# Performance work log

Measured on AMD Instinct MI355X. Metric: run time of the kernel, lower is better.

The kernel has to match this reference:

```python
import jax, jax.numpy as jnp
import numpy as np

B = 256
NO_A, NF_A = 64, 4   # class A: n_obj, n_field (all state fields)
NO_B, NF_B = 32, 3   # class B
NS = NF_A + NF_B     # total state fields = 7
DIN, DL, DG, DH = 128, 64, 64, 256
DGE = DG * NF_A + DG * NF_B          # 448 global encoding dim
DIN_A = DGE + DL * NF_A              # 704 decoder input dim, class A
DIN_B = DGE + DL * NF_B              # 640 decoder input dim, class B
NP = 2  # distribution params per field (mean, scale)


def lrelu(x):
    return jnp.where(x >= 0, x, 0.01 * x)


def setup_inputs() -> dict:
    key = jax.random.key(0)
    ks = iter(jax.random.split(key, 40))
    def rn(shape, s=1.0):
        return jax.random.normal(next(ks), shape, jnp.float32) * s
    def w(shape):
        return rn(shape, 0.05)
    def rb(shape):
        return jax.random.randint(next(ks), shape, 0, 2).astype(bool)
    inp = dict(
        x_A=rn((B, NO_A, NF_A, DIN)),
        x_B=rn((B, NO_B, NF_B, DIN)),
        global_mask=rb((B, NS, NF_A + NF_B)),
        local_mask_A=rb((B, NF_A, NF_A)),
        local_mask_B=rb((B, NF_B, NF_B)),
        objmask_A=rb((B, NO_A)),
        objmask_B=rb((B, NO_B)),
        enc_Wl_A=w((DIN, DL)), enc_bl_A=w((DL,)),
        enc_Wg_A=w((DIN, DG)), enc_bg_A=w((DG,)),
        enc_Wl_B=w((DIN, DL)), enc_bl_B=w((DL,)),
        enc_Wg_B=w((DIN, DG)), enc_bg_B=w((DG,)),
        dec_W1_A=w((NF_A, DIN_A, DH)), dec_b1_A=w((NF_A, DH)),
        dec_W2_A=w((NF_A, DH, DH)), dec_b2_A=w((NF_A, DH)),
        dec_Wp_A=w((NF_A, DH, NP)), dec_bp_A=w((NF_A, NP)),
        dec_W1_B=w((NF_B, DIN_B, DH)), dec_b1_B=w((NF_B, DH)),
        dec_W2_B=w((NF_B, DH, DH)), dec_b2_B=w((NF_B, DH)),
        dec_Wp_B=w((NF_B, DH, NP)), dec_bp_B=w((NF_B, NP)),
        rw_W1=w((DGE, DH)), rw_b1=w((DH,)),
        rw_W2=w((DH, DH)), rw_b2=w((DH,)),
        rw_W3=w((DH, 1)), rw_b3=w((1,)),
    )
    return inp


def encode_local(x, Wl, bl, attrmask):
    # x: (B, O, F, DIN) -> (B, O, S, F*DL), masked_retain over attrmask (B, S, F)
    h = jax.nn.relu(x @ Wl + bl)                                  # (B,O,F,DL)
    y = jnp.where(attrmask[:, None, :, :, None], h[:, :, None, :, :], 0.0)  # (B,O,S,F,DL)
    return y.reshape(y.shape[0], y.shape[1], y.shape[2], -1)


def encode_global(x, Wg, bg, attrmask, objmask):
    # x: (B, O, F, DIN), attrmask: (B, NS, F), objmask: (B, O)
    h = x @ Wg + bg                                               # (B,O,F,DG)
    h = jnp.where(objmask[:, :, None, None], h, 0.0)
    r = jax.nn.relu(jnp.sum(h, axis=1))                           # (B,F,DG) sum-pool over objects
    y = jnp.where(attrmask[:, :, :, None], r[:, None], 0.0)       # (B,NS,F,DG)
    y = jnp.concatenate([y, r[:, None]], axis=1)                  # (B,NS+1,F,DG)
    return y.reshape(y.shape[0], y.shape[1], -1)


def decode(x, W1, b1, W2, b2, Wp, bp):
    # x: (B, O, S, Din); per-field (s) decoders stacked on leading axis
    h = lrelu(jnp.einsum('bosi,sid->bosd', x, W1) + b1)
    h = lrelu(jnp.einsum('bosd,sde->bose', h, W2) + b2)
    return jnp.einsum('bose,sep->bosp', h, Wp) + bp               # (B,O,S,NP)


def reference(x_A, x_B, global_mask, local_mask_A, local_mask_B, objmask_A, objmask_B,
              enc_Wl_A, enc_bl_A, enc_Wg_A, enc_bg_A,
              enc_Wl_B, enc_bl_B, enc_Wg_B, enc_bg_B,
              dec_W1_A, dec_b1_A, dec_W2_A, dec_b2_A, dec_Wp_A, dec_bp_A,
              dec_W1_B, dec_b1_B, dec_W2_B, dec_b2_B, dec_Wp_B, dec_bp_B,
              rw_W1, rw_b1, rw_W2, rw_b2, rw_W3, rw_b3):
    g_A = encode_global(x_A, enc_Wg_A, enc_bg_A, global_mask[:, :, :NF_A], objmask_A)
    g_B = encode_global(x_B, enc_Wg_B, enc_bg_B, global_mask[:, :, NF_A:], objmask_B)
    G = jnp.concatenate([g_A, g_B], axis=2)                       # (B, NS+1, DGE)

    l_A = encode_local(x_A, enc_Wl_A, enc_bl_A, local_mask_A)     # (B,NO_A,NF_A,NF_A*DL)
    gs_A = jnp.broadcast_to(G[:, None, :NF_A, :], (B, NO_A, NF_A, DGE))
    out_A = decode(jnp.concatenate([l_A, gs_A], axis=3),
                   dec_W1_A, dec_b1_A, dec_W2_A, dec_b2_A, dec_Wp_A, dec_bp_A)

    l_B = encode_local(x_B, enc_Wl_B, enc_bl_B, local_mask_B)
    gs_B = jnp.broadcast_to(G[:, None, NF_A:NS, :], (B, NO_B, NF_B, DGE))
    out_B = decode(jnp.concatenate([l_B, gs_B], axis=3),
                   dec_W1_B, dec_b1_B, dec_W2_B, dec_b2_B, dec_Wp_B, dec_bp_B)

    h = lrelu(G[:, -1, :] @ rw_W1 + rw_b1)
    h = lrelu(h @ rw_W2 + rw_b2)
    reward = (h @ rw_W3 + rw_b3)[:, 0]                            # (B,)
    return out_A, out_B, reward
```

## Files before the change

kernel.cpp:

```cpp
#include <hip/hip_runtime.h>
#include <hip/hip_bf16.h>

constexpr int Bn   = 256;
constexpr int NOA  = 64, NFA = 4;
constexpr int NOB  = 32, NFB = 3;
constexpr int NS   = 7;
constexpr int DIN  = 128, DL = 64, DG = 64, DH = 256;
constexpr int DGE  = 448;
constexpr int DINA = 704;
constexpr int DINB = 640;

typedef short  short8v __attribute__((ext_vector_type(8)));
typedef float  f32x4   __attribute__((ext_vector_type(4)));

__device__ __forceinline__ unsigned short f2bf(float x) {
  union { float f; unsigned int u; } a; a.f = x;
  unsigned int r = a.u + 0x7fff + ((a.u >> 16) & 1);
  return (unsigned short)(r >> 16);
}


struct MidArgs {
  const float *xA, *xB, *WlA, *WlB, *blA, *blB;
  unsigned short *hlA, *hlB;
  const int *omA, *omB;
  const float *WgA, *bgA, *WgB, *bgB;
  float *rA, *rB;
  const float *W1A, *W1B, *W2A, *W2B;
  unsigned short *W1tA, *W1tB, *W1gtA, *W1gtB, *W2tA, *W2tB;
};

template<int F>
__device__ void hl_body(const float* __restrict__ x, const float* __restrict__ Wl,
                        const float* __restrict__ bl, unsigned short* __restrict__ hlf,
                        int m0, unsigned char* smem) {
  auto Asb = reinterpret_cast<unsigned short(*)[72]>(smem);
  auto Bsb = reinterpret_cast<unsigned short(*)[136]>(smem + 36864);
  float (*tile)[65] = reinterpret_cast<float(*)[65]>(smem);
  const int t = threadIdx.x, w = t >> 6, lane = t & 63;
  const int lr = lane & 15, lg = lane >> 4;
  constexpr int KB1 = 2 * F;

#pragma unroll
  for (int i = 0; i < 32; ++i) {
    int idx = t + i * 256;
    tile[idx >> 6][idx & 63] = Wl[idx];
  }
  __syncthreads();
#pragma unroll
  for (int i = 0; i < 32; ++i) {
    int idx = t + i * 256;
    int n = idx >> 7, k = idx & 127;
    Bsb[n][k] = f2bf(tile[k][n]);
  }
  __syncthreads();

  f32x4 acc[4][4] = {};
  for (int k0 = 0; k0 < DIN; k0 += 64) {
    const float* xp = x + (size_t)(m0 + t) * DIN + k0;
#pragma unroll
    for (int j = 0; j < 8; ++j) {
      float4 a = *(const float4*)(xp + j * 8);
      float4 b = *(const float4*)(xp + j * 8 + 4);
      union { short8v v; unsigned short e[8]; } u;
      u.e[0] = f2bf(a.x); u.e[1] = f2bf(a.y); u.e[2] = f2bf(a.z); u.e[3] = f2bf(a.w);
      u.e[4] = f2bf(b.x); u.e[5] = f2bf(b.y); u.e[6] = f2bf(b.z); u.e[7] = f2bf(b.w);
      *reinterpret_cast<short8v*>(&Asb[t][j * 8]) = u.v;
    }
#pragma unroll
    for (int ks = 0; ks < 2; ++ks) {
      short8v af[4], bf[4];
#pragma unroll
      for (int mi = 0; mi < 4; ++mi)
        af[mi] = *reinterpret_cast<const short8v*>(&Asb[w * 64 + mi * 16 + lr][ks * 32 + lg * 8]);
#pragma unroll
      for (int ni = 0; ni < 4; ++ni)
        bf[ni] = *reinterpret_cast<const short8v*>(&Bsb[ni * 16 + lr][k0 + ks * 32 + lg * 8]);
#pragma unroll
      for (int mi = 0; mi < 4; ++mi)
#pragma unroll
        for (int ni = 0; ni < 4; ++ni)
          acc[mi][ni] = __builtin_amdgcn_mfma_f32_16x16x32_bf16(
              af[mi], bf[ni], acc[mi][ni], 0, 0, 0);
    }
  }
#pragma unroll
  for (int mi = 0; mi < 4; ++mi)
#pragma unroll
    for (int ni = 0; ni < 4; ++ni)
#pragma unroll
      for (int reg = 0; reg < 4; ++reg) {
        int row = mi * 16 + lg * 4 + reg;
        int col = ni * 16 + lr;
        float v = fmaxf(acc[mi][ni][reg] + bl[col], 0.f);
        Asb[w * 64 + row][col] = f2bf(v);
      }
  const int mpb = m0 + w * 64;
#pragma unroll
  for (int j = 0; j < 8; ++j) {
    int c = lane + j * 64;
    int ml = c >> 3, dls = c & 7;
    int mp = mpb + ml;
    int mrow = mp / F, f = mp % F;
    int m6 = mrow >> 6, mi = (mrow >> 4) & 3, lr2 = mrow & 15;
    int kb = 2 * f + (dls >> 2), lg2 = dls & 3;
    size_t dst = ((((size_t)m6 * KB1 + kb) * 4 + mi) * 64 + (lg2 * 16 + lr2)) * 8;
    *reinterpret_cast<short8v*>(hlf + dst) =
        *reinterpret_cast<const short8v*>(&Asb[w * 64 + ml][dls * 8]);
  }
}

template<int O, int F>
__device__ void xsum_rg_body(const float* __restrict__ x, const int* __restrict__ om,
                             const float* __restrict__ Wg, const float* __restrict__ bg,
                             float* __restrict__ r, int b, unsigned char* smem) {
  float* xsm = reinterpret_cast<float*>(smem + 36864 + 17408);
  const int t = threadIdx.x, f = t >> 6, lane = t & 63;
  if (f >= F) return;
  unsigned long long bal = __ballot(lane < O && om[(size_t)b * O + lane] != 0);
  float cnt = (float)__popcll(bal);
  float a0 = 0.f, a1 = 0.f;
  const float* xb = x + ((size_t)b * O * F + f) * DIN + lane;
#pragma unroll 8
  for (int o = 0; o < O; ++o) {
    float m = (float)((bal >> o) & 1ull);
    a0 += m * xb[(size_t)o * F * DIN];
    a1 += m * xb[(size_t)o * F * DIN + 64];
  }
  xsm[f * 128 + lane] = a0;
  xsm[f * 128 + lane + 64] = a1;
  asm volatile("s_waitcnt lgkmcnt(0)" ::: "memory");
  float acc = 0.f;
  const float* wp = Wg + lane;
#pragma unroll 8
  for (int i = 0; i < DIN; ++i) acc += xsm[f * 128 + i] * wp[(size_t)i * DG];
  acc += cnt * bg[lane];
  r[((size_t)b * F + f) * DG + lane] = fmaxf(acc, 0.f);
}

__device__ void wtrans_tile(const float* __restrict__ src, unsigned short* __restrict__ dst,
                            int N, int DINc, int koff, int Kout,
                            int s, int kt, int nt, unsigned char* smem) {
  float (*tile)[65] = reinterpret_cast<float(*)[65]>(smem);
  const int t = threadIdx.x;
#pragma unroll
  for (int i = 0; i < 16; ++i) {
    int rr = (t >> 6) + i * 4, c = t & 63;
    tile[rr][c] = src[((size_t)s * DINc + koff + kt * 64 + rr) * N + nt * 64 + c];
  }
  __syncthreads();
#pragma unroll
  for (int i = 0; i < 2; ++i) {
    int cidx = t + i * 256;
    int n = cidx >> 3, kc = (cidx & 7) * 8;
    union { short8v v; unsigned short e[8]; } u;
#pragma unroll
    for (int j = 0; j < 8; ++j) u.e[j] = f2bf(tile[kc + j][n]);
    *reinterpret_cast<short8v*>(dst + ((size_t)s * N + nt * 64 + n) * Kout + kt * 64 + kc) = u.v;
  }
}

__device__ void wtrans_frag(const float* __restrict__ src, unsigned short* __restrict__ dst,
                            int DINc, int koff, int KB,
                            int s, int kt, int nt, unsigned char* smem) {
  float (*tile)[65] = reinterpret_cast<float(*)[65]>(smem);
  const int t = threadIdx.x;
#pragma unroll
  for (int i = 0; i < 16; ++i) {
    int rr = (t >> 6) + i * 4, c = t & 63;
    tile[rr][c] = src[((size_t)s * DINc + koff + kt * 64 + rr) * 256 + nt * 64 + c];
  }
  __syncthreads();
#pragma unroll
  for (int i = 0; i < 2; ++i) {
    int cidx = t + i * 256;
    int nl = cidx >> 3, kslot = cidx & 7;
    union { short8v v; unsigned short e[8]; } u;
#pragma unroll
    for (int j = 0; j < 8; ++j) u.e[j] = f2bf(tile[kslot * 8 + j][nl]);
    int kb = kt * 2 + (kslot >> 2);
    int lane = (kslot & 3) * 16 + (nl & 15);
    int nchunk = nt * 4 + (nl >> 4);
    *reinterpret_cast<short8v*>(
        dst + ((((size_t)s * KB + kb) * 16 + nchunk) * 64 + lane) * 8) = u.v;
  }
}

__global__ __launch_bounds__(256) void mid_kernel(MidArgs a) {
  __shared__ __align__(16) unsigned char smem[56320];
  const int bid = blockIdx.x;
  if (bid < 256) {
    hl_body<NFA>(a.xA, a.WlA, a.blA, a.hlA, bid * 256, smem);
    xsum_rg_body<NOA, NFA>(a.xA, a.omA, a.WgA, a.bgA, a.rA, bid, smem);
  } else if (bid < 352) {
    hl_body<NFB>(a.xB, a.WlB, a.blB, a.hlB, (bid - 256) * 256, smem);
  } else if (bid < 608) {
    xsum_rg_body<NOB, NFB>(a.xB, a.omB, a.WgB, a.bgB, a.rB, bid - 352, smem);
  } else {
    int r = bid - 608;
    if (r < 64)       { wtrans_frag(a.W1A, a.W1tA, DINA, 0, 8,
                                    r / 16, (r % 16) >> 2, r & 3, smem); }
    else if (r < 100) { r -= 64;  wtrans_frag(a.W1B, a.W1tB, DINB, 0, 6,
                                    r / 12, (r % 12) >> 2, r & 3, smem); }
    else if (r < 212) { r -= 100; wtrans_tile(a.W1A, a.W1gtA, 256, DINA, NFA * DL, DGE,
                                    r / 28, (r % 28) >> 2, r & 3, smem); }
    else if (r < 296) { r -= 212; wtrans_tile(a.W1B, a.W1gtB, 256, DINB, NFB * DL, DGE,
                                    r / 28, (r % 28) >> 2, r & 3, smem); }
    else if (r < 360) { r -= 296; wtrans_frag(a.W2A, a.W2tA, DH, 0, 8,
                                    r / 16, (r % 16) >> 2, r & 3, smem); }
    else              { r -= 360; wtrans_frag(a.W2B, a.W2tB, DH, 0, 8,
                                    r / 16, (r % 16) >> 2, r & 3, smem); }
  }
}

struct GprArgs {
  const float *rA, *rB; const int *gm;
  const unsigned short *W1gtA, *W1gtB;
  const float *b1A, *b1B;
  float *g1A, *g1B;
  const float *rwW1, *rwb1, *rwW2, *rwb2, *rwW3, *rwb3;
  float *outR;
};

__device__ void gpart_body(const GprArgs& a, int bx, int sg, unsigned char* smem) {
  auto Asb = reinterpret_cast<unsigned short(*)[72]>(smem);
  auto Bsb = reinterpret_cast<unsigned short(*)[72]>(smem + 9216);
  const int t = threadIdx.x, w = t >> 6, lane = t & 63;
  const int lr = lane & 15, lg = lane >> 4;
  const int m0 = bx * 64;
  const unsigned short* W1gt; const float* b1; float* g1; int S, sl;
  if (sg < NFA) { W1gt = a.W1gtA; b1 = a.b1A; g1 = a.g1A; S = NFA; sl = sg; }
  else          { W1gt = a.W1gtB; b1 = a.b1B; g1 = a.g1B; S = NFB; sl = sg - NFA; }

  f32x4 acc[4][4] = {};
  for (int kt = 0; kt < 7; ++kt) {
    __syncthreads();
    const int f = kt;
    const float* rsrc = (f < NFA) ? (a.rA + (size_t)f * DG) : (a.rB + (size_t)(f - NFA) * DG);
    const int rstride = (f < NFA) ? NFA * DG : NFB * DG;
#pragma unroll
    for (int i = 0; i < 2; ++i) {
      int c = t + i * 256;
      int row = c >> 3, kc = (c & 7) * 8;
      int b = m0 + row;
      float mk = (a.gm[((size_t)b * NS + sg) * NS + f] != 0) ? 1.f : 0.f;
      const float* rp = rsrc + (size_t)b * rstride + kc;
      union { short8v v; unsigned short e[8]; } u;
#pragma unroll
      for (int j = 0; j < 8; ++j) u.e[j] = f2bf(mk * rp[j]);
      *reinterpret_cast<short8v*>(&Asb[row][kc]) = u.v;
    }
#pragma unroll
    for (int i = 0; i < 8; ++i) {
      int c = t + i * 256;
      int n = c >> 3, kc = (c & 7) * 8;
      *reinterpret_cast<short8v*>(&Bsb[n][kc]) = *reinterpret_cast<const short8v*>(
          W1gt + ((size_t)sl * 256 + n) * DGE + kt * 64 + kc);
    }
    __syncthreads();
#pragma unroll
    for (int ks = 0; ks < 2; ++ks) {
      short8v af[4], bf[4];
#pragma unroll
      for (int mi = 0; mi < 4; ++mi)
        af[mi] = *reinterpret_cast<const short8v*>(&Asb[mi * 16 + lr][ks * 32 + lg * 8]);
#pragma unroll
      for (int ni = 0; ni < 4; ++ni)
        bf[ni] = *reinterpret_cast<const short8v*>(&Bsb[w * 64 + ni * 16 + lr][ks * 32 + lg * 8]);
#pragma unroll
      for (int mi = 0; mi < 4; ++mi)
#pragma unroll
        for (int ni = 0; ni < 4; ++ni)
          acc[mi][ni] = __builtin_amdgcn_mfma_f32_16x16x32_bf16(
              af[mi], bf[ni], acc[mi][ni], 0, 0, 0);
    }
  }
#pragma unroll
  for (int mi = 0; mi < 4; ++mi)
#pragma unroll
    for (int reg = 0; reg < 4; ++reg) {
      int b = m0 + mi * 16 + lg * 4 + reg;
#pragma unroll
      for (int ni = 0; ni < 4; ++ni) {
        int col = w * 64 + ni * 16 + lr;
        g1[((size_t)b * S + sl) * DH + col] = acc[mi][ni][reg] + b1[(size_t)sl * DH + col];
      }
    }
}

__device__ void reward_body(const GprArgs& a, int b, unsigned char* smem) {
  float* Gs = reinterpret_cast<float*>(smem);
  float* h1 = Gs + DGE;
  float* red = h1 + DH;
  const int t = threadIdx.x;
  for (int j = t; j < DGE; j += 256)
    Gs[j] = (j < NFA * DG) ? a.rA[((size_t)b * NFA + (j >> 6)) * DG + (j & 63)]
                           : a.rB[((size_t)b * NFB + ((j - NFA * DG) >> 6)) * DG + (j & 63)];
  __syncthreads();
  float acc = a.rwb1[t];
  for (int j = 0; j < DGE; ++j) acc += Gs[j] * a.rwW1[(size_t)j * DH + t];
  h1[t] = (acc >= 0.f) ? acc : 0.01f * acc;
  __syncthreads();
  acc = a.rwb2[t];
  for (int j = 0; j < DH; ++j) acc += h1[j] * a.rwW2[(size_t)j * DH + t];
  acc = (acc >= 0.f) ? acc : 0.01f * acc;
  red[t] = acc * a.rwW3[t];
  __syncthreads();
  for (int off = 128; off > 0; off >>= 1) {
    if (t < off) red[t] += red[t + off];
    __syncthreads();
  }
  if (t == 0) a.outR[b] = red[0] + a.rwb3[0];
}

__global__ __launch_bounds__(256) void gpr_kernel(GprArgs a) {
  __shared__ __align__(16) unsigned char smem[46080];
  const int bid = blockIdx.x;
  if (bid < 28) gpart_body(a, bid & 3, bid >> 2, smem);
  else          reward_body(a, bid - 28, smem);
}

struct DecArgs {
  const unsigned short *hlA, *hlB, *W1tA, *W1tB, *W2tA, *W2tB;
  const int *lmA, *lmB;
  const float *g1A, *g1B, *WpA, *WpB, *b2A, *b2B, *bpA, *bpB;
  float *outA, *outB;
};

template<int NO, int F>
__device__ __forceinline__ void dec_body(
    int mt, int s, unsigned short* h1s , float* red ,
    const unsigned short* __restrict__ hlf, const int* __restrict__ lm,
    const float* __restrict__ g1,
    const unsigned short* __restrict__ W1f, const unsigned short* __restrict__ W2f,
    const float* __restrict__ Wp, const float* __restrict__ b2,
    const float* __restrict__ bp, float* __restrict__ out) {
  constexpr int KB1 = 2 * F;
  const int t = threadIdx.x, w = t >> 6, lane = t & 63;
  const int lr = lane & 15, lg = lane >> 4;
  const int mh = w >> 2, nq = w & 3;
  const int m6 = mt * 2 + mh;
  const int m0 = mt * 128;

  unsigned mkl = 0, mkh = 0;
#pragma unroll
  for (int f = 0; f < F; ++f) {
    if (NO == 64) {
      unsigned bit = (lm[((size_t)m6 * F + s) * F + f] != 0) ? 1u : 0u;
      mkl |= bit << f; mkh |= bit << f;
    } else {
      int b0 = m6 * 2;
      if (lm[((size_t)b0 * F + s) * F + f])       mkl |= 1u << f;
      if (lm[((size_t)(b0 + 1) * F + s) * F + f]) mkh |= 1u << f;
    }
  }
  float g1r[2][4];
#pragma unroll
  for (int ni = 0; ni < 4; ++ni) {
    int col = nq * 64 + ni * 16 + lr;
    if (NO == 64) {
      g1r[0][ni] = g1[((size_t)m6 * F + s) * DH + col];
      g1r[1][ni] = g1r[0][ni];
    } else {
      g1r[0][ni] = g1[((size_t)(m6 * 2) * F + s) * DH + col];
      g1r[1][ni] = g1[((size_t)(m6 * 2 + 1) * F + s) * DH + col];
    }
  }

  f32x4 acc[4][4] = {};
  const short8v zero8 = {0, 0, 0, 0, 0, 0, 0, 0};

  const unsigned short* Afb = hlf + (size_t)m6 * KB1 * 2048 + lane * 8;
  const unsigned short* B1b = W1f + ((size_t)s * KB1 * 16 + nq * 4) * 512 + lane * 8;
#pragma unroll
  for (int kb = 0; kb < KB1; ++kb) {
    const int f = kb >> 1;
    const bool okl = (mkl >> f) & 1, okh = (mkh >> f) & 1;
    const unsigned short* ab = Afb + (size_t)kb * 2048;
    const unsigned short* bb = B1b + (size_t)kb * 8192;
    short8v af[4], bf[4];
#pragma unroll
    for (int mi = 0; mi < 4; ++mi) {
      const bool ok = (mi < 2) ? okl : okh;
      const unsigned short* p = ok ? (ab + mi * 512) : bb;
      af[mi] = *reinterpret_cast<const short8v*>(p);
    }
#pragma unroll
    for (int ni = 0; ni < 4; ++ni)
      bf[ni] = *reinterpret_cast<const short8v*>(bb + ni * 512);
#pragma unroll
    for (int mi = 0; mi < 4; ++mi) {
      const bool ok = (mi < 2) ? okl : okh;
      af[mi] = ok ? af[mi] : zero8;
    }
#pragma unroll
    for (int mi = 0; mi < 4; ++mi)
#pragma unroll
      for (int ni = 0; ni < 4; ++ni)
        acc[mi][ni] = __builtin_amdgcn_mfma_f32_16x16x32_bf16(
            af[mi], bf[ni], acc[mi][ni], 0, 0, 0);
  }

#pragma unroll
  for (int mi = 0; mi < 4; ++mi) {
    int gi = (NO == 32) ? (mi >> 1) : 0;
#pragma unroll
    for (int reg = 0; reg < 4; ++reg) {
      int row = mh * 64 + mi * 16 + lg * 4 + reg;
#pragma unroll
      for (int ni = 0; ni < 4; ++ni) {
        int col = nq * 64 + ni * 16 + lr;
        float v = acc[mi][ni][reg] + g1r[gi][ni];
        v = (v >= 0.f) ? v : 0.01f * v;
        h1s[row * 264 + col] = f2bf(v);
        acc[mi][ni][reg] = 0.f;
      }
    }
  }
  __syncthreads();

  const unsigned short* B2b = W2f + ((size_t)s * 8 * 16 + nq * 4) * 512 + lane * 8;
#pragma unroll
  for (int kb = 0; kb < 8; ++kb) {
    short8v af[4], bf[4];
#pragma unroll
    for (int mi = 0; mi < 4; ++mi)
      af[mi] = *reinterpret_cast<const short8v*>(
          h1s + (mh * 64 + mi * 16 + lr) * 264 + kb * 32 + lg * 8);
#pragma unroll
    for (int ni = 0; ni < 4; ++ni)
      bf[ni] = *reinterpret_cast<const short8v*>(B2b + (size_t)kb * 8192 + ni * 512);
#pragma unroll
    for (int mi = 0; mi < 4; ++mi)
#pragma unroll
      for (int ni = 0; ni < 4; ++ni)
        acc[mi][ni] = __builtin_amdgcn_mfma_f32_16x16x32_bf16(
            af[mi], bf[ni], acc[mi][ni], 0, 0, 0);
  }

  float part[4][4][2] = {};
  const float* Wps = Wp + (size_t)s * DH * 2;
  const float* b2s = b2 + (size_t)s * DH;
#pragma unroll
  for (int ni = 0; ni < 4; ++ni) {
    int col = nq * 64 + ni * 16 + lr;
    float wp0 = Wps[col * 2 + 0], wp1 = Wps[col * 2 + 1], bb2 = b2s[col];
#pragma unroll
    for (int mi = 0; mi < 4; ++mi)
#pragma unroll
      for (int reg = 0; reg < 4; ++reg) {
        float v = acc[mi][ni][reg] + bb2;
        v = (v >= 0.f) ? v : 0.01f * v;
        part[mi][reg][0] += v * wp0;
        part[mi][reg][1] += v * wp1;
      }
  }
#pragma unroll
  for (int off = 1; off < 16; off <<= 1)
#pragma unroll
    for (int mi = 0; mi < 4; ++mi)
#pragma unroll
      for (int reg = 0; reg < 4; ++reg) {
        part[mi][reg][0] += __shfl_xor(part[mi][reg][0], off, 64);
        part[mi][reg][1] += __shfl_xor(part[mi][reg][1], off, 64);
      }
  if (lr == 0)
#pragma unroll
    for (int mi = 0; mi < 4; ++mi)
#pragma unroll
      for (int reg = 0; reg < 4; ++reg) {
        int rowin = mi * 16 + lg * 4 + reg;
        red[((size_t)w * 64 + rowin) * 2 + 0] = part[mi][reg][0];
        red[((size_t)w * 64 + rowin) * 2 + 1] = part[mi][reg][1];
      }
  __syncthreads();
  if (t < 256) {
    int row = t >> 1, p = t & 1;
    int mhr = row >> 6, rowin = row & 63;
    float sum = 0.f;
#pragma unroll
    for (int q = 0; q < 4; ++q)
      sum += red[((size_t)(mhr * 4 + q) * 64 + rowin) * 2 + p];
    out[((size_t)(m0 + row) * F + s) * 2 + p] = sum + bp[(size_t)s * 2 + p];
  }
}

__global__ __launch_bounds__(512, 4) void dec_kernel(DecArgs a) {
  __shared__ __align__(16) unsigned short h1s[128 * 264];
  __shared__ float red[1024];
  const int bid = blockIdx.x;
  if (bid < 512) {
    dec_body<NOA, NFA>(bid & 127, bid >> 7, h1s, red, a.hlA, a.lmA, a.g1A,
                       a.W1tA, a.W2tA, a.WpA, a.b2A, a.bpA, a.outA);
  } else {
    int r = bid - 512;
    dec_body<NOB, NFB>(r & 63, r >> 6, h1s, red, a.hlB, a.lmB, a.g1B,
                       a.W1tB, a.W2tB, a.WpB, a.b2B, a.bpB, a.outB);
  }
}

extern "C" void kernel_launch(void* const* d_in, const int* in_sizes, int n_in,
                              void* d_out, int out_size, void* d_ws, size_t ws_size,
                              hipStream_t stream) {
  const float* x_A  = (const float*)d_in[0];
  const float* x_B  = (const float*)d_in[1];
  const int*   gm   = (const int*)d_in[2];
  const int*   lmA  = (const int*)d_in[3];
  const int*   lmB  = (const int*)d_in[4];
  const int*   omA  = (const int*)d_in[5];
  const int*   omB  = (const int*)d_in[6];
  const float* Wl_A = (const float*)d_in[7];
  const float* bl_A = (const float*)d_in[8];
  const float* Wg_A = (const float*)d_in[9];
  const float* bg_A = (const float*)d_in[10];
  const float* Wl_B = (const float*)d_in[11];
  const float* bl_B = (const float*)d_in[12];
  const float* Wg_B = (const float*)d_in[13];
  const float* bg_B = (const float*)d_in[14];
  const float* W1_A = (const float*)d_in[15];
  const float* b1_A = (const float*)d_in[16];
  const float* W2_A = (const float*)d_in[17];
  const float* b2_A = (const float*)d_in[18];
  const float* Wp_A = (const float*)d_in[19];
  const float* bp_A = (const float*)d_in[20];
  const float* W1_B = (const float*)d_in[21];
  const float* b1_B = (const float*)d_in[22];
  const float* W2_B = (const float*)d_in[23];
  const float* b2_B = (const float*)d_in[24];
  const float* Wp_B = (const float*)d_in[25];
  const float* bp_B = (const float*)d_in[26];
  const float* rwW1 = (const float*)d_in[27];
  const float* rwb1 = (const float*)d_in[28];
  const float* rwW2 = (const float*)d_in[29];
  const float* rwb2 = (const float*)d_in[30];
  const float* rwW3 = (const float*)d_in[31];
  const float* rwb3 = (const float*)d_in[32];

  float* ws   = (float*)d_ws;
  float* rA   = ws;
  float* rB   = rA + 65536;
  float* g1A  = rB + 49152;
  float* g1B  = g1A + 262144;
  unsigned short* us    = (unsigned short*)(g1B + 196608);
  unsigned short* hlA   = us;
  unsigned short* hlB   = hlA + 4194304;
  unsigned short* W1tA  = hlB + 1572864;
  unsigned short* W1tB  = W1tA + 262144;
  unsigned short* W2tA  = W1tB + 147456;
  unsigned short* W2tB  = W2tA + 262144;
  unsigned short* W1gtA = W2tB + 196608;
  unsigned short* W1gtB = W1gtA + 458752;

  float* outA = (float*)d_out;
  float* outB = outA + 131072;
  float* outR = outA + 180224;

  MidArgs m;
  m.xA = x_A; m.xB = x_B; m.WlA = Wl_A; m.WlB = Wl_B; m.blA = bl_A; m.blB = bl_B;
  m.hlA = hlA; m.hlB = hlB; m.omA = omA; m.omB = omB;
  m.WgA = Wg_A; m.bgA = bg_A; m.WgB = Wg_B; m.bgB = bg_B;
  m.rA = rA; m.rB = rB;
  m.W1A = W1_A; m.W1B = W1_B; m.W2A = W2_A; m.W2B = W2_B;
  m.W1tA = W1tA; m.W1tB = W1tB; m.W1gtA = W1gtA; m.W1gtB = W1gtB;
  m.W2tA = W2tA; m.W2tB = W2tB;

  GprArgs g;
  g.rA = rA; g.rB = rB; g.gm = gm; g.W1gtA = W1gtA; g.W1gtB = W1gtB;
  g.b1A = b1_A; g.b1B = b1_B; g.g1A = g1A; g.g1B = g1B;
  g.rwW1 = rwW1; g.rwb1 = rwb1; g.rwW2 = rwW2; g.rwb2 = rwb2;
  g.rwW3 = rwW3; g.rwb3 = rwb3; g.outR = outR;

  DecArgs d;
  d.hlA = hlA; d.hlB = hlB; d.W1tA = W1tA; d.W1tB = W1tB;
  d.W2tA = W2tA; d.W2tB = W2tB; d.lmA = lmA; d.lmB = lmB;
  d.g1A = g1A; d.g1B = g1B; d.WpA = Wp_A; d.WpB = Wp_B;
  d.b2A = b2_A; d.b2B = b2_B; d.bpA = bp_A; d.bpB = bp_B;
  d.outA = outA; d.outB = outB;

  mid_kernel<<<1016, 256, 0, stream>>>(m);
  gpr_kernel<<<284, 256, 0, stream>>>(g);
  dec_kernel<<<704, 512, 0, stream>>>(d);
}
```

Before: 88.80 us.

## Stage decoder GEMM1 tiles via direct global-to-LDS loads and halve h1 buffer

The first decoder GEMM now stages its A and B tiles into shared memory with global_load_lds, so the eight waves share one copy of the W1 tile instead of each loading its own fragments from global memory. The second GEMM is split into two phases, one per half of the waves, so the h1 staging buffer only needs 64 rows and total LDS per block shrinks. This aims to cut redundant global traffic and raise occupancy. In exchange it adds a __syncthreads per k-step and leaves half the waves idle in each GEMM2 phase, which serialises that stage.

```diff
diff --git a/kernel.cpp b/kernel.cpp
--- a/kernel.cpp
+++ b/kernel.cpp
@@ -17,6 +17,12 @@
   union { float f; unsigned int u; } a; a.f = x;
   unsigned int r = a.u + 0x7fff + ((a.u >> 16) & 1);
   return (unsigned short)(r >> 16);
+}
+
+__device__ __forceinline__ void gload_lds16(const void* g, void* l) {
+  __builtin_amdgcn_global_load_lds(
+      (const __attribute__((address_space(1))) void*)g,
+      (__attribute__((address_space(3))) void*)l, 16, 0, 0);
 }
 
 
@@ -329,7 +335,9 @@
 
 template<int NO, int F>
 __device__ __forceinline__ void dec_body(
-    int mt, int s, unsigned short* h1s , float* red ,
+    int mt, int s,
+    unsigned short* h1s , unsigned short* Ast ,
+    unsigned short* Bst ,
     const unsigned short* __restrict__ hlf, const int* __restrict__ lm,
     const float* __restrict__ g1,
     const unsigned short* __restrict__ W1f, const unsigned short* __restrict__ W2f,
@@ -370,74 +378,83 @@
   f32x4 acc[4][4] = {};
   const short8v zero8 = {0, 0, 0, 0, 0, 0, 0, 0};
 
-  const unsigned short* Afb = hlf + (size_t)m6 * KB1 * 2048 + lane * 8;
-  const unsigned short* B1b = W1f + ((size_t)s * KB1 * 16 + nq * 4) * 512 + lane * 8;
+  const int m6s = mt * 2 + (t >> 8);
 #pragma unroll
   for (int kb = 0; kb < KB1; ++kb) {
+    gload_lds16(hlf + ((size_t)m6s * KB1 + kb) * 2048 + (t & 255) * 8, Ast + t * 8);
+    const unsigned short* bbase = W1f + ((size_t)s * KB1 + kb) * 8192;
+    gload_lds16(bbase + t * 8,         Bst + t * 8);
+    gload_lds16(bbase + (t + 512) * 8, Bst + (t + 512) * 8);
+    __syncthreads();
+
     const int f = kb >> 1;
     const bool okl = (mkl >> f) & 1, okh = (mkh >> f) & 1;
-    const unsigned short* ab = Afb + (size_t)kb * 2048;
-    const unsigned short* bb = B1b + (size_t)kb * 8192;
     short8v af[4], bf[4];
 #pragma unroll
-    for (int mi = 0; mi < 4; ++mi) {
-      const bool ok = (mi < 2) ? okl : okh;
-      const unsigned short* p = ok ? (ab + mi * 512) : bb;
-      af[mi] = *reinterpret_cast<const short8v*>(p);
-    }
-#pragma unroll
-    for (int ni = 0; ni < 4; ++ni)
-      bf[ni] = *reinterpret_cast<const short8v*>(bb + ni * 512);
+    for (int mi = 0; mi < 4; ++mi)
+      af[mi] = *reinterpret_cast<const short8v*>(Ast + mh * 2048 + mi * 512 + lane * 8);
 #pragma unroll
     for (int mi = 0; mi < 4; ++mi) {
       const bool ok = (mi < 2) ? okl : okh;
       af[mi] = ok ? af[mi] : zero8;
     }
 #pragma unroll
+    for (int ni = 0; ni < 4; ++ni)
+      bf[ni] = *reinterpret_cast<const short8v*>(Bst + ((nq * 4 + ni) * 64 + lane) * 8);
+#pragma unroll
     for (int mi = 0; mi < 4; ++mi)
 #pragma unroll
       for (int ni = 0; ni < 4; ++ni)
         acc[mi][ni] = __builtin_amdgcn_mfma_f32_16x16x32_bf16(
             af[mi], bf[ni], acc[mi][ni], 0, 0, 0);
-  }
-
-#pragma unroll
-  for (int mi = 0; mi < 4; ++mi) {
-    int gi = (NO == 32) ? (mi >> 1) : 0;
-#pragma unroll
-    for (int reg = 0; reg < 4; ++reg) {
-      int row = mh * 64 + mi * 16 + lg * 4 + reg;
-#pragma unroll
-      for (int ni = 0; ni < 4; ++ni) {
-        int col = nq * 64 + ni * 16 + lr;
-        float v = acc[mi][ni][reg] + g1r[gi][ni];
-        v = (v >= 0.f) ? v : 0.01f * v;
-        h1s[row * 264 + col] = f2bf(v);
-        acc[mi][ni][reg] = 0.f;
+    __syncthreads();
+  }
+
+  const unsigned short* B2b = W2f + ((size_t)s * 8 * 16 + nq * 4) * 512 + lane * 8;
+#pragma unroll
+  for (int ph = 0; ph < 2; ++ph) {
+    if (mh == ph) {
+#pragma unroll
+      for (int mi = 0; mi < 4; ++mi) {
+        int gi = (NO == 32) ? (mi >> 1) : 0;
+#pragma unroll
+        for (int reg = 0; reg < 4; ++reg) {
+          int lrow = mi * 16 + lg * 4 + reg;
+#pragma unroll
+          for (int ni = 0; ni < 4; ++ni) {
+            int col = nq * 64 + ni * 16 + lr;
+            float v = acc[mi][ni][reg] + g1r[gi][ni];
+            v = (v >= 0.f) ? v : 0.01f * v;
+            h1s[lrow * 264 + col] = f2bf(v);
+            acc[mi][ni][reg] = 0.f;
+          }
+        }
       }
     }
-  }
-  __syncthreads();
-
-  const unsigned short* B2b = W2f + ((size_t)s * 8 * 16 + nq * 4) * 512 + lane * 8;
-#pragma unroll
-  for (int kb = 0; kb < 8; ++kb) {
-    short8v af[4], bf[4];
-#pragma unroll
-    for (int mi = 0; mi < 4; ++mi)
-      af[mi] = *reinterpret_cast<const short8v*>(
-          h1s + (mh * 64 + mi * 16 + lr) * 264 + kb * 32 + lg * 8);
-#pragma unroll
-    for (int ni = 0; ni < 4; ++ni)
-      bf[ni] = *reinterpret_cast<const short8v*>(B2b + (size_t)kb * 8192 + ni * 512);
-#pragma unroll
-    for (int mi = 0; mi < 4; ++mi)
-#pragma unroll
-      for (int ni = 0; ni < 4; ++ni)
-        acc[mi][ni] = __builtin_amdgcn_mfma_f32_16x16x32_bf16(
-            af[mi], bf[ni], acc[mi][ni], 0, 0, 0);
-  }
-
+    __syncthreads();
+    if (mh == ph) {
+#pragma unroll
+      for (int kb = 0; kb < 8; ++kb) {
+        short8v af[4], bf[4];
+#pragma unroll
+        for (int mi = 0; mi < 4; ++mi)
+          af[mi] = *reinterpret_cast<const short8v*>(
+              h1s + (mi * 16 + lr) * 264 + kb * 32 + lg * 8);
+#pragma unroll
+        for (int ni = 0; ni < 4; ++ni)
+          bf[ni] = *reinterpret_cast<const short8v*>(B2b + (size_t)kb * 8192 + ni * 512);
+#pragma unroll
+        for (int mi = 0; mi < 4; ++mi)
+#pragma unroll
+          for (int ni = 0; ni < 4; ++ni)
+            acc[mi][ni] = __builtin_amdgcn_mfma_f32_16x16x32_bf16(
+                af[mi], bf[ni], acc[mi][ni], 0, 0, 0);
+      }
+    }
+    __syncthreads();
+  }
+
+  float* red = reinterpret_cast<float*>(Ast);
   float part[4][4][2] = {};
   const float* Wps = Wp + (size_t)s * DH * 2;
   const float* b2s = b2 + (size_t)s * DH;
@@ -486,15 +503,16 @@
 }
 
 __global__ __launch_bounds__(512, 4) void dec_kernel(DecArgs a) {
-  __shared__ __align__(16) unsigned short h1s[128 * 264];
-  __shared__ float red[1024];
+  __shared__ __align__(16) unsigned short h1s[64 * 264];
+  __shared__ __align__(16) unsigned short Ast[4096];
+  __shared__ __align__(16) unsigned short Bst[8192];
   const int bid = blockIdx.x;
   if (bid < 512) {
-    dec_body<NOA, NFA>(bid & 127, bid >> 7, h1s, red, a.hlA, a.lmA, a.g1A,
+    dec_body<NOA, NFA>(bid & 127, bid >> 7, h1s, Ast, Bst, a.hlA, a.lmA, a.g1A,
                        a.W1tA, a.W2tA, a.WpA, a.b2A, a.bpA, a.outA);
   } else {
     int r = bid - 512;
-    dec_body<NOB, NFB>(r & 63, r >> 6, h1s, red, a.hlB, a.lmB, a.g1B,
+    dec_body<NOB, NFB>(r & 63, r >> 6, h1s, Ast, Bst, a.hlB, a.lmB, a.g1B,
                        a.W1tB, a.W2tB, a.WpB, a.b2B, a.bpB, a.outB);
   }
 }
```

New measurement: 99.68 us. 1.12x slower.
